# Performance work log

Hardware: AMD Instinct MI355X
Metric: run time of the kernel (lower is better)

Reference implementation:

```python
import jax, jax.numpy as jnp
import numpy as np

K = 2        # top-k experts
ALPHA = 0.01  # load-balance loss weight
BETA = 0.1    # z-router loss weight

B, T, D, E = 4, 4096, 2048, 64


def setup_inputs() -> dict:
    key = jax.random.key(0)
    kx, kw = jax.random.split(key)
    x = jax.random.normal(kx, (B, T, D), dtype=jnp.float32)
    W = jax.random.normal(kw, (D, E), dtype=jnp.float32) * (1.0 / np.sqrt(D))
    b = jnp.zeros((E,), dtype=jnp.float32)
    return {"x": x, "W": W, "b": b}


def reference(x, W, b):
    # Router logits and softmax: [B, T, E]
    logits = jnp.einsum("btd,de->bte", x, W) + b
    scores = jax.nn.softmax(logits, axis=-1)

    # Top-k selection and renormalized combine weights: [B, T, K]
    topk_vals, topk_idx = jax.lax.top_k(scores, K)
    combine = topk_vals / jnp.sum(topk_vals, axis=-1, keepdims=True)

    # Load-balance loss (Fedus et al. 2022): f_e = fraction of tokens whose
    # max score is expert e; P_e = mean prob mass on expert e.
    is_max = (scores == jnp.max(scores, axis=-1, keepdims=True)).astype(jnp.float32)
    f = jnp.mean(is_max, axis=(0, 1))   # [E]
    P = jnp.mean(scores, axis=(0, 1))   # [E]
    balance_loss = ALPHA * jnp.mean(f * P)

    # Z-router loss; faithfully applied to post-softmax scores as in source.
    lse = jax.nn.logsumexp(scores, axis=-1)  # [B, T]
    z_loss = BETA * jnp.mean(lse ** 2)

    return topk_idx, combine, balance_loss, z_loss
```

## Files before the change

kernel.cpp:

```cpp
#include <hip/hip_runtime.h>
#include <math.h>

#define NTOK 16384
#define DDIM 2048
#define NEXP 64
#define MT   16
#define KCH  128
#define NCH  (DDIM / KCH)

#define ACC_N  129
#define WF_OFF 256
#define VSTRIDE ((size_t)4 * 64 * 64 * 8)

typedef __attribute__((ext_vector_type(8))) short short8_t;
typedef __attribute__((ext_vector_type(4))) float f32x4;

__device__ __forceinline__ unsigned short f2bf(float f) {
    unsigned int u = __float_as_uint(f);
    u += 0x7fffu + ((u >> 16) & 1u);
    return (unsigned short)(u >> 16);
}
__device__ __forceinline__ float bf2f(unsigned short s) {
    return __uint_as_float(((unsigned int)s) << 16);
}

__global__ __launch_bounds__(256) void prep(
    const float* __restrict__ W, float* __restrict__ ws)
{
    const int i = blockIdx.x * 256 + threadIdx.x;
    if (blockIdx.x == 0 && threadIdx.x < ACC_N) ws[threadIdx.x] = 0.0f;
    const int k = i >> 6, e = i & 63;
    const float v = W[i];
    unsigned short h = f2bf(v);
    float r1 = v - bf2f(h);
    unsigned short m = f2bf(r1);
    unsigned short l = f2bf(r1 - bf2f(m));
    unsigned short* wf = (unsigned short*)(ws + WF_OFF);
    const int g = e >> 4, ks = k >> 5;
    const int lane = (((k >> 3) & 3) << 4) | (e & 15);
    const int j = k & 7;
    const size_t base = ((((size_t)g * 64) + ks) * 64 + lane) * 8 + j;
    wf[base] = h;
    wf[VSTRIDE + base] = m;
    wf[2 * VSTRIDE + base] = l;
}

__global__ __launch_bounds__(256, 4) void gate_fused(
    const float* __restrict__ x, const unsigned short* __restrict__ wf,
    const float* __restrict__ bias, float* __restrict__ out,
    float* __restrict__ acc_g)
{
    __shared__ __align__(16) unsigned short xh[2][MT * KCH];
    __shared__ __align__(16) unsigned short xm_[2][MT * KCH];
    __shared__ __align__(16) unsigned short xl_[2][MT * KCH];
    __shared__ float logits[MT][68];
    __shared__ int   f_loc[NEXP];
    __shared__ float p_loc[NEXP];
    __shared__ float z_loc;

    const int tid  = threadIdx.x;
    const int tok0 = blockIdx.x * MT;
    const int lane = tid & 63;
    const int g    = __builtin_amdgcn_readfirstlane(tid >> 6);
    const int phase = (blockIdx.x & 3) * 4;

    if (tid < NEXP) { f_loc[tid] = 0; p_loc[tid] = 0.0f; }
    if (tid == 0) z_loc = 0.0f;

    const int srow = tid >> 4;
    const int scg  = tid & 15;
    const float* xs = x + (size_t)(tok0 + srow) * DDIM + scg * 8;
    const int wbase = srow * KCH;
    const int s0 = (scg ^ (srow & 7)) * 8;

    const int arow  = lane & 15;
    const int akq   = lane >> 4;
    const int abase = arow * KCH;

    f32x4 acc0 = {0.f, 0.f, 0.f, 0.f};
    f32x4 acc1 = {0.f, 0.f, 0.f, 0.f};
    f32x4 acc2 = {0.f, 0.f, 0.f, 0.f};

    {
        const float* x0 = xs + phase * KCH;
        float4 a0 = *(const float4*)(x0 + 0);
        float4 a1 = *(const float4*)(x0 + 4);
        float xv[8];
        *(float4*)&xv[0] = a0; *(float4*)&xv[4] = a1;
        unsigned short th[8], tm[8], tl[8];
        #pragma unroll
        for (int i = 0; i < 8; ++i) {
            float f = xv[i];
            th[i] = f2bf(f);
            float r = f - bf2f(th[i]);
            tm[i] = f2bf(r);
            tl[i] = f2bf(r - bf2f(tm[i]));
        }
        *(short8_t*)&xh[0][wbase + s0]  = *(short8_t*)&th[0];
        *(short8_t*)&xm_[0][wbase + s0] = *(short8_t*)&tm[0];
        *(short8_t*)&xl_[0][wbase + s0] = *(short8_t*)&tl[0];
    }
    const float* xp1 = xs + ((phase + 1) & (NCH - 1)) * KCH;
    float4 pv0 = *(const float4*)(xp1 + 0);
    float4 pv1 = *(const float4*)(xp1 + 4);

    #pragma unroll 1
    for (int c = 0; c < NCH; ++c) {
        __syncthreads();
        const int cb = c & 1, nb = cb ^ 1;
        const int actual = (phase + c) & (NCH - 1);

        const unsigned short* wb0 =
            wf + ((((size_t)g * 64) + actual * 4) * 64 + lane) * 8;
        short8_t B[12];
        #pragma unroll
        for (int s = 0; s < 4; ++s) {
            const unsigned short* wb = wb0 + (size_t)s * 64 * 8;
            B[s * 3 + 0] = *(const short8_t*)&wb[0];
            B[s * 3 + 1] = *(const short8_t*)&wb[VSTRIDE];
            B[s * 3 + 2] = *(const short8_t*)&wb[2 * VSTRIDE];
        }

        if (c + 1 < NCH) {
            float xv[8];
            *(float4*)&xv[0] = pv0; *(float4*)&xv[4] = pv1;
            unsigned short th[8], tm[8], tl[8];
            #pragma unroll
            for (int i = 0; i < 8; ++i) {
                float f = xv[i];
                th[i] = f2bf(f);
                float r = f - bf2f(th[i]);
                tm[i] = f2bf(r);
                tl[i] = f2bf(r - bf2f(tm[i]));
            }
            *(short8_t*)&xh[nb][wbase + s0]  = *(short8_t*)&th[0];
            *(short8_t*)&xm_[nb][wbase + s0] = *(short8_t*)&tm[0];
            *(short8_t*)&xl_[nb][wbase + s0] = *(short8_t*)&tl[0];
            if (c + 2 < NCH) {
                const float* xn = xs + ((phase + c + 2) & (NCH - 1)) * KCH;
                pv0 = *(const float4*)(xn + 0);
                pv1 = *(const float4*)(xn + 4);
            }
        }

        #pragma unroll
        for (int i = 0; i < 12; ++i)
            asm volatile("" :: "v"(B[i]));

        __builtin_amdgcn_s_setprio(1);
        #pragma unroll
        for (int s = 0; s < 4; ++s) {
            const int slot = (((s * 4 + akq) ^ (arow & 7))) * 8;
            short8_t ah = *(const short8_t*)&xh[cb][abase + slot];
            short8_t am = *(const short8_t*)&xm_[cb][abase + slot];
            short8_t al = *(const short8_t*)&xl_[cb][abase + slot];
            acc0 = __builtin_amdgcn_mfma_f32_16x16x32_bf16(ah, B[s*3+0], acc0, 0, 0, 0);
            acc1 = __builtin_amdgcn_mfma_f32_16x16x32_bf16(ah, B[s*3+1], acc1, 0, 0, 0);
            acc2 = __builtin_amdgcn_mfma_f32_16x16x32_bf16(am, B[s*3+1], acc2, 0, 0, 0);
            acc0 = __builtin_amdgcn_mfma_f32_16x16x32_bf16(ah, B[s*3+2], acc0, 0, 0, 0);
            acc1 = __builtin_amdgcn_mfma_f32_16x16x32_bf16(am, B[s*3+0], acc1, 0, 0, 0);
            acc2 = __builtin_amdgcn_mfma_f32_16x16x32_bf16(al, B[s*3+0], acc2, 0, 0, 0);
        }
        __builtin_amdgcn_s_setprio(0);
    }

    #pragma unroll
    for (int r = 0; r < 4; ++r)
        logits[akq * 4 + r][g * 16 + arow] = (acc0[r] + acc1[r]) + acc2[r];
    __syncthreads();

    const int tx = tid & 15;
    const int tg = tid >> 4;
    const int e0 = tx * 4;
    const int gt = tok0 + tg;

    float bb[4];
    *(float4*)bb = *(const float4*)&bias[e0];
    float l[4];
    {
        float4 lv = *(const float4*)&logits[tg][e0];
        l[0] = lv.x + bb[0]; l[1] = lv.y + bb[1];
        l[2] = lv.z + bb[2]; l[3] = lv.w + bb[3];
    }

    float v1 = l[0], v2 = -INFINITY;
    int   i1 = e0,   i2 = 0x7fffffff;
    #pragma unroll
    for (int j = 1; j < 4; ++j) {
        float v = l[j]; int e = e0 + j;
        if (v > v1)      { v2 = v1; i2 = i1; v1 = v; i1 = e; }
        else if (v > v2) { v2 = v;  i2 = e; }
    }
    #pragma unroll
    for (int off = 1; off < 16; off <<= 1) {
        float o1 = __shfl_xor(v1, off, 16); int oi1 = __shfl_xor(i1, off, 16);
        float o2 = __shfl_xor(v2, off, 16); int oi2 = __shfl_xor(i2, off, 16);
        if (o1 > v1 || (o1 == v1 && oi1 < i1)) {
            float cs = v1; int ci = i1;
            v1 = o1; i1 = oi1;
            if (cs > o2 || (cs == o2 && ci < oi2)) { v2 = cs; i2 = ci;  }
            else                                   { v2 = o2; i2 = oi2; }
        } else {
            if (o1 > v2 || (o1 == v2 && oi1 < i2)) { v2 = o1; i2 = oi1; }
        }
    }
    const float mx = v1;

    float sden[4], dsum = 0.0f;
    #pragma unroll
    for (int j = 0; j < 4; ++j) { sden[j] = __expf(l[j] - mx); dsum += sden[j]; }
    #pragma unroll
    for (int off = 1; off < 16; off <<= 1) dsum += __shfl_xor(dsum, off, 16);
    const float inv = 1.0f / dsum;

    float p[4], zsum = 0.0f;
    #pragma unroll
    for (int j = 0; j < 4; ++j) {
        p[j] = sden[j] * inv;
        zsum += __expf(p[j]);
    }
    #pragma unroll
    for (int off = 1; off < 16; off <<= 1) zsum += __shfl_xor(zsum, off, 16);

    float zacc = 0.0f;
    if (tx == 0) {
        const float s2 = __expf(v2 - mx);
        const float ci = 1.0f / (1.0f + s2);
        out[2 * gt]     = (float)i1;
        out[2 * gt + 1] = (float)i2;
        out[2 * NTOK + 2 * gt]     = ci;
        out[2 * NTOK + 2 * gt + 1] = s2 * ci;
        atomicAdd(&f_loc[i1], 1);
        float lse = __logf(zsum);
        zacc = lse * lse;
    }

    #pragma unroll
    for (int off = 1; off < 64; off <<= 1) zacc += __shfl_xor(zacc, off);
    if ((tid & 63) == 0) atomicAdd(&z_loc, zacc);

    #pragma unroll
    for (int j = 0; j < 4; ++j) {
        p[j] += __shfl_xor(p[j], 16);
        p[j] += __shfl_xor(p[j], 32);
    }
    if ((tid & 63) < 16) {
        #pragma unroll
        for (int j = 0; j < 4; ++j) atomicAdd(&p_loc[e0 + j], p[j]);
    }

    __syncthreads();
    if (tid < NEXP) {
        atomicAdd(&acc_g[64 + tid], p_loc[tid]);
        if (f_loc[tid]) atomicAdd(&acc_g[tid], (float)f_loc[tid]);
    }
    if (tid == 0) atomicAdd(&acc_g[128], z_loc);
}

__global__ void gate_finalize(const float* __restrict__ acc, float* __restrict__ out) {
    int e = threadIdx.x;
    float v = acc[e] * acc[64 + e];
    #pragma unroll
    for (int off = 32; off > 0; off >>= 1) v += __shfl_down(v, off);
    if (e == 0) {
        const float NT = (float)NTOK;
        out[2 * NTOK * 2]     = 0.01f * (v / (float)NEXP) / (NT * NT);
        out[2 * NTOK * 2 + 1] = 0.1f * acc[128] / NT;
    }
}

extern "C" void kernel_launch(void* const* d_in, const int* in_sizes, int n_in,
                              void* d_out, int out_size, void* d_ws, size_t ws_size,
                              hipStream_t stream) {
    const float* x    = (const float*)d_in[0];
    const float* W    = (const float*)d_in[1];
    const float* bias = (const float*)d_in[2];
    float* out = (float*)d_out;
    float* ws  = (float*)d_ws;
    const unsigned short* wfrag = (const unsigned short*)(ws + WF_OFF);

    prep<<<(DDIM * NEXP) / 256, 256, 0, stream>>>(W, ws);
    gate_fused<<<NTOK / MT, 256, 0, stream>>>(x, wfrag, bias, out, ws);
    gate_finalize<<<1, 64, 0, stream>>>(ws, out);
}
```

Baseline: 69.76 us.

## Split router GEMM along D into two partial kernels with separate epilogue

The fused kernel is split into a GEMM kernel that runs two K-halves per token tile (twice the blocks) and writes partial logits to workspace. A new epilogue kernel sums the two partials, adds bias, and does the softmax/top-k/loss accumulation over 64 tokens per block. The aim is more parallelism and occupancy (launch bounds raised to 6) for the memory-bound GEMM, at the cost of an extra launch and 8 MB of partial-logit round trips. The phase-staggered chunk ordering and the register-pinning asm barrier are also removed.

```diff
diff --git a/kernel.cpp b/kernel.cpp
--- a/kernel.cpp
+++ b/kernel.cpp
@@ -5,11 +5,14 @@
 #define DDIM 2048
 #define NEXP 64
 #define MT   16
+#define KSPLIT 2
+#define KRANGE (DDIM / KSPLIT)
 #define KCH  128
-#define NCH  (DDIM / KCH)
-
-#define ACC_N  129
-#define WF_OFF 256
+#define NCH  (KRANGE / KCH)
+
+#define ACC_N   129
+#define PART_OFF 256
+#define WF_OFF  (PART_OFF + KSPLIT * NTOK * NEXP)
 #define VSTRIDE ((size_t)4 * 64 * 64 * 8)
 
 typedef __attribute__((ext_vector_type(8))) short short8_t;
@@ -45,31 +48,26 @@
     wf[2 * VSTRIDE + base] = l;
 }
 
-__global__ __launch_bounds__(256, 4) void gate_fused(
+__global__ __launch_bounds__(256, 6) void gate_part(
     const float* __restrict__ x, const unsigned short* __restrict__ wf,
-    const float* __restrict__ bias, float* __restrict__ out,
-    float* __restrict__ acc_g)
+    float* __restrict__ pws)
 {
     __shared__ __align__(16) unsigned short xh[2][MT * KCH];
     __shared__ __align__(16) unsigned short xm_[2][MT * KCH];
     __shared__ __align__(16) unsigned short xl_[2][MT * KCH];
-    __shared__ float logits[MT][68];
-    __shared__ int   f_loc[NEXP];
-    __shared__ float p_loc[NEXP];
-    __shared__ float z_loc;
 
     const int tid  = threadIdx.x;
-    const int tok0 = blockIdx.x * MT;
+    const int tb   = blockIdx.x & 1023;
+    const int sp   = blockIdx.x >> 10;
+    const int tok0 = tb * MT;
+    const int kb   = sp * KRANGE;
+
     const int lane = tid & 63;
     const int g    = __builtin_amdgcn_readfirstlane(tid >> 6);
-    const int phase = (blockIdx.x & 3) * 4;
-
-    if (tid < NEXP) { f_loc[tid] = 0; p_loc[tid] = 0.0f; }
-    if (tid == 0) z_loc = 0.0f;
 
     const int srow = tid >> 4;
     const int scg  = tid & 15;
-    const float* xs = x + (size_t)(tok0 + srow) * DDIM + scg * 8;
+    const float* xs = x + (size_t)(tok0 + srow) * DDIM + kb + scg * 8;
     const int wbase = srow * KCH;
     const int s0 = (scg ^ (srow & 7)) * 8;
 
@@ -82,9 +80,8 @@
     f32x4 acc2 = {0.f, 0.f, 0.f, 0.f};
 
     {
-        const float* x0 = xs + phase * KCH;
-        float4 a0 = *(const float4*)(x0 + 0);
-        float4 a1 = *(const float4*)(x0 + 4);
+        float4 a0 = *(const float4*)(xs + 0);
+        float4 a1 = *(const float4*)(xs + 4);
         float xv[8];
         *(float4*)&xv[0] = a0; *(float4*)&xv[4] = a1;
         unsigned short th[8], tm[8], tl[8];
@@ -100,18 +97,18 @@
         *(short8_t*)&xm_[0][wbase + s0] = *(short8_t*)&tm[0];
         *(short8_t*)&xl_[0][wbase + s0] = *(short8_t*)&tl[0];
     }
-    const float* xp1 = xs + ((phase + 1) & (NCH - 1)) * KCH;
-    float4 pv0 = *(const float4*)(xp1 + 0);
-    float4 pv1 = *(const float4*)(xp1 + 4);
+    float4 pv0 = *(const float4*)(xs + KCH + 0);
+    float4 pv1 = *(const float4*)(xs + KCH + 4);
+
+    const int ks0 = kb >> 5;
 
     #pragma unroll 1
     for (int c = 0; c < NCH; ++c) {
         __syncthreads();
         const int cb = c & 1, nb = cb ^ 1;
-        const int actual = (phase + c) & (NCH - 1);
 
         const unsigned short* wb0 =
-            wf + ((((size_t)g * 64) + actual * 4) * 64 + lane) * 8;
+            wf + ((((size_t)g * 64) + ks0 + c * 4) * 64 + lane) * 8;
         short8_t B[12];
         #pragma unroll
         for (int s = 0; s < 4; ++s) {
@@ -137,15 +134,11 @@
             *(short8_t*)&xm_[nb][wbase + s0] = *(short8_t*)&tm[0];
             *(short8_t*)&xl_[nb][wbase + s0] = *(short8_t*)&tl[0];
             if (c + 2 < NCH) {
-                const float* xn = xs + ((phase + c + 2) & (NCH - 1)) * KCH;
+                const float* xn = xs + (c + 2) * KCH;
                 pv0 = *(const float4*)(xn + 0);
                 pv1 = *(const float4*)(xn + 4);
             }
         }
-
-        #pragma unroll
-        for (int i = 0; i < 12; ++i)
-            asm volatile("" :: "v"(B[i]));
 
         __builtin_amdgcn_s_setprio(1);
         #pragma unroll
@@ -164,75 +157,103 @@
         __builtin_amdgcn_s_setprio(0);
     }
 
+    float* pb = pws + ((size_t)sp * NTOK + tok0) * NEXP;
     #pragma unroll
     for (int r = 0; r < 4; ++r)
-        logits[akq * 4 + r][g * 16 + arow] = (acc0[r] + acc1[r]) + acc2[r];
+        pb[(size_t)(akq * 4 + r) * NEXP + g * 16 + arow] =
+            (acc0[r] + acc1[r]) + acc2[r];
+}
+
+#define ETOK 64
+
+__global__ __launch_bounds__(256) void epilogue(
+    const float* __restrict__ pws, const float* __restrict__ bias,
+    float* __restrict__ out, float* __restrict__ acc_g)
+{
+    __shared__ int   f_loc[NEXP];
+    __shared__ float p_loc[NEXP];
+    __shared__ float z_loc;
+
+    const int tid = threadIdx.x;
+    const int tx  = tid & 15;
+    const int tg  = tid >> 4;
+    const int e0  = tx * 4;
+
+    if (tid < NEXP) { f_loc[tid] = 0; p_loc[tid] = 0.0f; }
+    if (tid == 0) z_loc = 0.0f;
     __syncthreads();
-
-    const int tx = tid & 15;
-    const int tg = tid >> 4;
-    const int e0 = tx * 4;
-    const int gt = tok0 + tg;
 
     float bb[4];
     *(float4*)bb = *(const float4*)&bias[e0];
-    float l[4];
-    {
-        float4 lv = *(const float4*)&logits[tg][e0];
-        l[0] = lv.x + bb[0]; l[1] = lv.y + bb[1];
-        l[2] = lv.z + bb[2]; l[3] = lv.w + bb[3];
-    }
-
-    float v1 = l[0], v2 = -INFINITY;
-    int   i1 = e0,   i2 = 0x7fffffff;
-    #pragma unroll
-    for (int j = 1; j < 4; ++j) {
-        float v = l[j]; int e = e0 + j;
-        if (v > v1)      { v2 = v1; i2 = i1; v1 = v; i1 = e; }
-        else if (v > v2) { v2 = v;  i2 = e; }
-    }
-    #pragma unroll
-    for (int off = 1; off < 16; off <<= 1) {
-        float o1 = __shfl_xor(v1, off, 16); int oi1 = __shfl_xor(i1, off, 16);
-        float o2 = __shfl_xor(v2, off, 16); int oi2 = __shfl_xor(i2, off, 16);
-        if (o1 > v1 || (o1 == v1 && oi1 < i1)) {
-            float cs = v1; int ci = i1;
-            v1 = o1; i1 = oi1;
-            if (cs > o2 || (cs == o2 && ci < oi2)) { v2 = cs; i2 = ci;  }
-            else                                   { v2 = o2; i2 = oi2; }
-        } else {
-            if (o1 > v2 || (o1 == v2 && oi1 < i2)) { v2 = o1; i2 = oi1; }
-        }
-    }
-    const float mx = v1;
-
-    float sden[4], dsum = 0.0f;
-    #pragma unroll
-    for (int j = 0; j < 4; ++j) { sden[j] = __expf(l[j] - mx); dsum += sden[j]; }
-    #pragma unroll
-    for (int off = 1; off < 16; off <<= 1) dsum += __shfl_xor(dsum, off, 16);
-    const float inv = 1.0f / dsum;
-
-    float p[4], zsum = 0.0f;
-    #pragma unroll
-    for (int j = 0; j < 4; ++j) {
-        p[j] = sden[j] * inv;
-        zsum += __expf(p[j]);
-    }
-    #pragma unroll
-    for (int off = 1; off < 16; off <<= 1) zsum += __shfl_xor(zsum, off, 16);
-
+
+    float pacc[4] = {0.f, 0.f, 0.f, 0.f};
     float zacc = 0.0f;
-    if (tx == 0) {
-        const float s2 = __expf(v2 - mx);
-        const float ci = 1.0f / (1.0f + s2);
-        out[2 * gt]     = (float)i1;
-        out[2 * gt + 1] = (float)i2;
-        out[2 * NTOK + 2 * gt]     = ci;
-        out[2 * NTOK + 2 * gt + 1] = s2 * ci;
-        atomicAdd(&f_loc[i1], 1);
-        float lse = __logf(zsum);
-        zacc = lse * lse;
+
+    for (int it = 0; it < ETOK / 16; ++it) {
+        const int gt = blockIdx.x * ETOK + it * 16 + tg;
+
+        float l[4];
+        {
+            const size_t ro = (size_t)gt * NEXP + e0;
+            float4 q0 = *(const float4*)&pws[ro];
+            float4 q1 = *(const float4*)&pws[(size_t)NTOK * NEXP + ro];
+            l[0] = (q0.x + q1.x) + bb[0];
+            l[1] = (q0.y + q1.y) + bb[1];
+            l[2] = (q0.z + q1.z) + bb[2];
+            l[3] = (q0.w + q1.w) + bb[3];
+        }
+
+        float v1 = l[0], v2 = -INFINITY;
+        int   i1 = e0,   i2 = 0x7fffffff;
+        #pragma unroll
+        for (int j = 1; j < 4; ++j) {
+            float v = l[j]; int e = e0 + j;
+            if (v > v1)      { v2 = v1; i2 = i1; v1 = v; i1 = e; }
+            else if (v > v2) { v2 = v;  i2 = e; }
+        }
+        #pragma unroll
+        for (int off = 1; off < 16; off <<= 1) {
+            float o1 = __shfl_xor(v1, off, 16); int oi1 = __shfl_xor(i1, off, 16);
+            float o2 = __shfl_xor(v2, off, 16); int oi2 = __shfl_xor(i2, off, 16);
+            if (o1 > v1 || (o1 == v1 && oi1 < i1)) {
+                float cs = v1; int ci = i1;
+                v1 = o1; i1 = oi1;
+                if (cs > o2 || (cs == o2 && ci < oi2)) { v2 = cs; i2 = ci;  }
+                else                                   { v2 = o2; i2 = oi2; }
+            } else {
+                if (o1 > v2 || (o1 == v2 && oi1 < i2)) { v2 = o1; i2 = oi1; }
+            }
+        }
+        const float mx = v1;
+
+        float sden[4], dsum = 0.0f;
+        #pragma unroll
+        for (int j = 0; j < 4; ++j) { sden[j] = __expf(l[j] - mx); dsum += sden[j]; }
+        #pragma unroll
+        for (int off = 1; off < 16; off <<= 1) dsum += __shfl_xor(dsum, off, 16);
+        const float inv = 1.0f / dsum;
+
+        float zsum = 0.0f;
+        #pragma unroll
+        for (int j = 0; j < 4; ++j) {
+            float pj = sden[j] * inv;
+            pacc[j] += pj;
+            zsum += __expf(pj);
+        }
+        #pragma unroll
+        for (int off = 1; off < 16; off <<= 1) zsum += __shfl_xor(zsum, off, 16);
+
+        if (tx == 0) {
+            const float s2 = __expf(v2 - mx);
+            const float ci = 1.0f / (1.0f + s2);
+            out[2 * gt]     = (float)i1;
+            out[2 * gt + 1] = (float)i2;
+            out[2 * NTOK + 2 * gt]     = ci;
+            out[2 * NTOK + 2 * gt + 1] = s2 * ci;
+            atomicAdd(&f_loc[i1], 1);
+            float lse = __logf(zsum);
+            zacc += lse * lse;
+        }
     }
 
     #pragma unroll
@@ -241,12 +262,12 @@
 
     #pragma unroll
     for (int j = 0; j < 4; ++j) {
-        p[j] += __shfl_xor(p[j], 16);
-        p[j] += __shfl_xor(p[j], 32);
+        pacc[j] += __shfl_xor(pacc[j], 16);
+        pacc[j] += __shfl_xor(pacc[j], 32);
     }
     if ((tid & 63) < 16) {
         #pragma unroll
-        for (int j = 0; j < 4; ++j) atomicAdd(&p_loc[e0 + j], p[j]);
+        for (int j = 0; j < 4; ++j) atomicAdd(&p_loc[e0 + j], pacc[j]);
     }
 
     __syncthreads();
@@ -277,9 +298,11 @@
     const float* bias = (const float*)d_in[2];
     float* out = (float*)d_out;
     float* ws  = (float*)d_ws;
+    float* pws = ws + PART_OFF;
     const unsigned short* wfrag = (const unsigned short*)(ws + WF_OFF);
 
     prep<<<(DDIM * NEXP) / 256, 256, 0, stream>>>(W, ws);
-    gate_fused<<<NTOK / MT, 256, 0, stream>>>(x, wfrag, bias, out, ws);
+    gate_part<<<KSPLIT * (NTOK / MT), 256, 0, stream>>>(x, wfrag, pws);
+    epilogue<<<NTOK / ETOK, 256, 0, stream>>>(pws, bias, out, ws);
     gate_finalize<<<1, 64, 0, stream>>>(ws, out);
 }
```

Result: slower. 81.91 us (+17.4%).
